# Optimization experiments

Measured on AMD Instinct MI355X. Metric: run time of the kernel, lower is better.

## Reference

```python
import jax, jax.numpy as jnp
import numpy as np

N_NODES = 50000
N_EDGES = 1_600_000
IN_C, HID_C, OUT_C = 512, 256, 50
ALPHA = 0.1
NUM_LAYERS = 10


def setup_inputs() -> dict:
    key = jax.random.key(0)
    ks = jax.random.split(key, 8)
    x = jax.random.normal(ks[0], (N_NODES, IN_C), dtype=jnp.float32)
    edge_row = jax.random.randint(ks[1], (N_EDGES,), 0, N_NODES, dtype=jnp.int32)
    edge_col = jax.random.randint(ks[2], (N_EDGES,), 0, N_NODES, dtype=jnp.int32)
    edge_weight = jax.random.uniform(ks[3], (N_EDGES,), dtype=jnp.float32)
    s1 = 1.0 / np.sqrt(IN_C)
    s2 = 1.0 / np.sqrt(HID_C)
    W1 = jax.random.uniform(ks[4], (IN_C, HID_C), minval=-s1, maxval=s1, dtype=jnp.float32)
    b1 = jax.random.uniform(ks[5], (HID_C,), minval=-s1, maxval=s1, dtype=jnp.float32)
    W2 = jax.random.uniform(ks[6], (HID_C, OUT_C), minval=-s2, maxval=s2, dtype=jnp.float32)
    b2 = jax.random.uniform(ks[7], (OUT_C,), minval=-s2, maxval=s2, dtype=jnp.float32)
    return {"x": x, "edge_row": edge_row, "edge_col": edge_col,
            "edge_weight": edge_weight, "W1": W1, "b1": b1, "W2": W2, "b2": b2}


def reference(x, edge_row, edge_col, edge_weight, W1, b1, W2, b2):
    # MLP: Linear -> ReLU -> Linear (dropout inactive in eval, no batch norm)
    h = jax.nn.relu(x @ W1 + b1)          # [N, HID_C]
    h = h @ W2 + b2                        # [N, OUT_C]
    x0 = h

    def spmm(v):
        # out[i] = sum_{e: row[e]==i} w[e] * v[col[e]]
        msgs = v[edge_col] * edge_weight[:, None]   # [E, OUT_C]
        return jax.ops.segment_sum(msgs, edge_row, num_segments=N_NODES)

    def step(h, _):
        h = spmm(h) * (1.0 - ALPHA) + ALPHA * x0
        return h, None

    h, _ = jax.lax.scan(step, h, None, length=NUM_LAYERS)
    return jax.nn.log_softmax(h, axis=1)
```

## Files before the change

kernel.cpp:

```cpp
#include <hip/hip_runtime.h>
#include <cstddef>
#include <cstdint>
#include <math.h>

#define N_NODES 50000
#define N_EDGES 1600000
#define IN_C 512
#define HID_C 256
#define OUT_C 50
#define PAD_C 64
#define NUM_LAYERS 10
#define NBUCK 98
#define BSHIFT 9
#define BCAP 20480
#define PHB_CHUNK 8192
#define PHB_BLOCKS 196

typedef __attribute__((ext_vector_type(8))) short short8;
typedef __attribute__((ext_vector_type(4))) float floatx4;

__device__ inline unsigned short f2bf(float f) {
    unsigned int u = __float_as_uint(f);
    u += 0x7fffu + ((u >> 16) & 1u);
    return (unsigned short)(u >> 16);
}

#define ASYNC16(g, l)                                                     \
    __builtin_amdgcn_global_load_lds(                                     \
        (const __attribute__((address_space(1))) void*)(g),               \
        (__attribute__((address_space(3))) void*)(l), 16, 0, 0)

__global__ __launch_bounds__(256) void transpose_w1(const float* __restrict__ W1,
                                                    unsigned short* __restrict__ Wt) {
    __shared__ float tile[32][33];
    int bx = blockIdx.x;
    int by = blockIdx.y;
    int tx = threadIdx.x & 31, ty = threadIdx.x >> 5;
#pragma unroll
    for (int i = 0; i < 32; i += 8)
        tile[ty + i][tx] = W1[(bx * 32 + ty + i) * HID_C + by * 32 + tx];
    __syncthreads();
#pragma unroll
    for (int i = 0; i < 32; i += 8)
        Wt[(size_t)(by * 32 + ty + i) * IN_C + bx * 32 + tx] = f2bf(tile[tx][ty + i]);
}

__global__ __launch_bounds__(256) void gemm1_mfma(const float* __restrict__ A,
                                                  const unsigned short* __restrict__ Wt,
                                                  const float* __restrict__ bias,
                                                  float* __restrict__ C) {
    __shared__ float          As[2][64 * 32];
    __shared__ unsigned short Bs[2][256 * 32];
    const int tid  = threadIdx.x;
    const int wave = tid >> 6, lane = tid & 63;
    const int quad = lane >> 4, l16 = lane & 15;
    const int m0 = blockIdx.x * 64;
    const int wm = (wave >> 1) * 32;
    const int wn = (wave & 1) * 128;

    floatx4 acc[2][8];
#pragma unroll
    for (int i = 0; i < 2; ++i)
#pragma unroll
        for (int j = 0; j < 8; ++j) acc[i][j] = (floatx4){0.f, 0.f, 0.f, 0.f};

    auto stage = [&](int buf, int k0) {
#pragma unroll
        for (int j = 0; j < 2; ++j) {
            int slot = tid + j * 256;
            int r = slot >> 3, c = slot & 7;
            int gr = m0 + r;
            if (gr >= N_NODES) gr = N_NODES - 1;
            const float* src = A + (size_t)gr * IN_C + k0 + ((c ^ (r & 7)) << 2);
            ASYNC16(src, &As[buf][slot << 2]);
        }
#pragma unroll
        for (int j = 0; j < 4; ++j) {
            int slot = tid + j * 256;
            int n = slot >> 2, c = slot & 3;
            const unsigned short* src = Wt + (size_t)n * IN_C + k0 + (c << 3);
            ASYNC16(src, &Bs[buf][slot << 3]);
        }
    };

    auto compute = [&](int buf) {
        short8 bfr[8], afr[2];
#pragma unroll
        for (int nt = 0; nt < 8; ++nt) {
            int n = wn + nt * 16 + l16;
            bfr[nt] = *(const short8*)&Bs[buf][(n << 5) + (quad << 3)];
        }
#pragma unroll
        for (int mt = 0; mt < 2; ++mt) {
            int r  = wm + mt * 16 + l16;
            int rx = r & 7;
            float4 lo = *(const float4*)&As[buf][(r << 5) + (((2 * quad)     ^ rx) << 2)];
            float4 hi = *(const float4*)&As[buf][(r << 5) + (((2 * quad + 1) ^ rx) << 2)];
            short8 a;
            a[0] = (short)f2bf(lo.x); a[1] = (short)f2bf(lo.y);
            a[2] = (short)f2bf(lo.z); a[3] = (short)f2bf(lo.w);
            a[4] = (short)f2bf(hi.x); a[5] = (short)f2bf(hi.y);
            a[6] = (short)f2bf(hi.z); a[7] = (short)f2bf(hi.w);
            afr[mt] = a;
        }
#pragma unroll
        for (int mt = 0; mt < 2; ++mt)
#pragma unroll
            for (int nt = 0; nt < 8; ++nt)
                acc[mt][nt] = __builtin_amdgcn_mfma_f32_16x16x32_bf16(afr[mt], bfr[nt],
                                                                      acc[mt][nt], 0, 0, 0);
    };

    stage(0, 0);
    __syncthreads();
    int buf = 0;
    for (int ks = 0; ks < IN_C / 32; ++ks) {
        if (ks + 1 < IN_C / 32) stage(buf ^ 1, (ks + 1) * 32);
        compute(buf);
        __syncthreads();
        buf ^= 1;
    }

#pragma unroll
    for (int nt = 0; nt < 8; ++nt) {
        int n = wn + nt * 16 + l16;
        float bn = bias[n];
#pragma unroll
        for (int mt = 0; mt < 2; ++mt) {
#pragma unroll
            for (int r = 0; r < 4; ++r) {
                int m = m0 + wm + mt * 16 + quad * 4 + r;
                if (m < N_NODES) {
                    float v = acc[mt][nt][r] + bn;
                    C[(size_t)m * HID_C + n] = v > 0.f ? v : 0.f;
                }
            }
        }
    }
}

__global__ void pad_w2(const float* __restrict__ W2, const float* __restrict__ b2,
                       float* __restrict__ Wp, float* __restrict__ bp) {
    int idx = blockIdx.x * blockDim.x + threadIdx.x;
    if (idx < HID_C * PAD_C) {
        int k = idx >> 6, j = idx & 63;
        Wp[idx] = (j < OUT_C) ? W2[k * OUT_C + j] : 0.f;
    }
    if (idx < PAD_C) bp[idx] = (idx < OUT_C) ? b2[idx] : 0.f;
}

__global__ __launch_bounds__(256) void gemm2_tiled(const float* __restrict__ H,
                                                   const float* __restrict__ Wp,
                                                   const float* __restrict__ bp,
                                                   float* __restrict__ h0f,
                                                   unsigned short* __restrict__ h0b) {
    __shared__ float As[16][68];
    __shared__ float Bs[16][64];
    const int tid = threadIdx.x;
    const int tx = tid & 15;
    const int ty = tid >> 4;
    const int m0 = blockIdx.x * 64;

    float acc[4][4];
#pragma unroll
    for (int i = 0; i < 4; ++i)
#pragma unroll
        for (int j = 0; j < 4; ++j) acc[i][j] = 0.f;

    const int arow = tid >> 2;
    const int akk  = (tid & 3) << 2;
    const int brow = tid >> 4;
    const int bcol = (tid & 15) << 2;

    for (int k0 = 0; k0 < HID_C; k0 += 16) {
        float4 av = make_float4(0.f, 0.f, 0.f, 0.f);
        int gr = m0 + arow;
        if (gr < N_NODES)
            av = *(const float4*)(H + (size_t)gr * HID_C + k0 + akk);
        As[akk + 0][arow] = av.x;
        As[akk + 1][arow] = av.y;
        As[akk + 2][arow] = av.z;
        As[akk + 3][arow] = av.w;
        float4 bv = *(const float4*)(Wp + (size_t)(k0 + brow) * PAD_C + bcol);
        *(float4*)&Bs[brow][bcol] = bv;
        __syncthreads();

#pragma unroll
        for (int kk = 0; kk < 16; ++kk) {
            float a[4], b[4];
#pragma unroll
            for (int i = 0; i < 4; ++i) a[i] = As[kk][ty * 4 + i];
#pragma unroll
            for (int j = 0; j < 4; ++j) b[j] = Bs[kk][tx * 4 + j];
#pragma unroll
            for (int i = 0; i < 4; ++i)
#pragma unroll
                for (int j = 0; j < 4; ++j) acc[i][j] = fmaf(a[i], b[j], acc[i][j]);
        }
        __syncthreads();
    }

#pragma unroll
    for (int i = 0; i < 4; ++i) {
        int r = m0 + ty * 4 + i;
        if (r >= N_NODES) continue;
#pragma unroll
        for (int j = 0; j < 4; ++j) {
            int c = tx * 4 + j;
            float v = acc[i][j] + bp[c];
            h0f[(size_t)r * PAD_C + c] = v;
            h0b[(size_t)r * PAD_C + c] = f2bf(v);
        }
    }
}

__global__ __launch_bounds__(256) void bucket_scatter(const int* __restrict__ erow,
                                                      const int* __restrict__ ecol,
                                                      const float* __restrict__ ew,
                                                      int* __restrict__ bfill,
                                                      uint2* __restrict__ buckets) {
    __shared__ int lcnt[NBUCK];
    __shared__ int lbase[NBUCK];
    const int t = threadIdx.x;
    for (int b = t; b < NBUCK; b += 256) lcnt[b] = 0;
    __syncthreads();
    const int e0 = blockIdx.x * PHB_CHUNK;
    const int e1 = min(e0 + PHB_CHUNK, N_EDGES);
    for (int e = e0 + t; e < e1; e += 256)
        atomicAdd(&lcnt[erow[e] >> BSHIFT], 1);
    __syncthreads();
    for (int b = t; b < NBUCK; b += 256) {
        lbase[b] = atomicAdd(&bfill[b], lcnt[b]);
        lcnt[b] = 0;
    }
    __syncthreads();
    for (int e = e0 + t; e < e1; e += 256) {
        int r = erow[e];
        int b = r >> BSHIFT;
        int o = atomicAdd(&lcnt[b], 1);
        int idx = lbase[b] + o;
        if (idx < BCAP) {
            unsigned packed = ((unsigned)(r - (b << BSHIFT)) << 17) | (unsigned)ecol[e];
            buckets[(size_t)b * BCAP + idx] = make_uint2(packed, __float_as_uint(ew[e]));
        }
    }
}

__global__ __launch_bounds__(128) void bucket_scan(const int* __restrict__ bfill,
                                                   int* __restrict__ bbase,
                                                   int* __restrict__ rowptr) {
    __shared__ int sd[128];
    int t = threadIdx.x;
    int v = (t < NBUCK) ? min(bfill[t], BCAP) : 0;
    sd[t] = v;
    __syncthreads();
    for (int off = 1; off < 128; off <<= 1) {
        int x = (t >= off) ? sd[t - off] : 0;
        __syncthreads();
        sd[t] += x;
        __syncthreads();
    }
    if (t < NBUCK) bbase[t] = sd[t] - v;
    if (t == NBUCK - 1) {
        bbase[NBUCK] = sd[t];
        rowptr[N_NODES] = sd[t];
    }
}

__global__ __launch_bounds__(256) void bucket_csr(const uint2* __restrict__ buckets,
                                                  const int* __restrict__ bfill,
                                                  const int* __restrict__ bbase,
                                                  int* __restrict__ rowptr,
                                                  uint2* __restrict__ edges) {
    __shared__ int hist[512];
    __shared__ int excl[512];
    __shared__ int psum[256];
    const int b = blockIdx.x;
    const int t = threadIdx.x;
    const int n = min(bfill[b], BCAP);
    const uint2* bk = buckets + (size_t)b * BCAP;

    hist[t] = 0; hist[t + 256] = 0;
    __syncthreads();
    for (int i = t; i < n; i += 256)
        atomicAdd(&hist[bk[i].x >> 17], 1);
    __syncthreads();
    int a0 = hist[2 * t], a1 = hist[2 * t + 1];
    psum[t] = a0 + a1;
    __syncthreads();
    for (int off = 1; off < 256; off <<= 1) {
        int x = (t >= off) ? psum[t - off] : 0;
        __syncthreads();
        psum[t] += x;
        __syncthreads();
    }
    int pe = psum[t] - (a0 + a1);
    excl[2 * t] = pe;
    excl[2 * t + 1] = pe + a0;
    __syncthreads();
    const int base = bbase[b];
#pragma unroll
    for (int k = 0; k < 2; ++k) {
        int lr = t + k * 256;
        int r = (b << BSHIFT) + lr;
        if (r < N_NODES) rowptr[r] = base + excl[lr];
    }
    hist[t] = 0; hist[t + 256] = 0;
    __syncthreads();
    for (int i = t; i < n; i += 256) {
        uint2 ed = bk[i];
        int lr = ed.x >> 17;
        int pos = base + excl[lr] + atomicAdd(&hist[lr], 1);
        edges[pos] = make_uint2(ed.x & 0x1FFFFu, ed.y);
    }
}

template <bool LAST>
__global__ __launch_bounds__(256) void prop8(const int* __restrict__ rowptr,
                                             const uint2* __restrict__ edges,
                                             const unsigned short* __restrict__ hin,
                                             const float* __restrict__ h0f,
                                             unsigned short* __restrict__ hout_b,
                                             float* __restrict__ out_f) {
    int wid = (blockIdx.x * blockDim.x + threadIdx.x) >> 6;
    if (wid >= N_NODES) return;
    int lane = threadIdx.x & 63;
    int slot = lane >> 3;
    int lc   = lane & 7;
    int s = rowptr[wid], e = rowptr[wid + 1];

    float acc0[8], acc1[8];
#pragma unroll
    for (int k = 0; k < 8; ++k) { acc0[k] = 0.f; acc1[k] = 0.f; }

    int i = s;
    for (; i + 16 <= e; i += 16) {
        uint2 cw0 = edges[i + slot];
        uint2 cw1 = edges[i + 8 + slot];
        uint4 hv0 = *(const uint4*)((const char*)hin + ((size_t)cw0.x << 7) + lc * 16);
        uint4 hv1 = *(const uint4*)((const char*)hin + ((size_t)cw1.x << 7) + lc * 16);
        float w0 = __uint_as_float(cw0.y);
        float w1 = __uint_as_float(cw1.y);
        acc0[0] = fmaf(w0, __uint_as_float(hv0.x << 16),         acc0[0]);
        acc0[1] = fmaf(w0, __uint_as_float(hv0.x & 0xffff0000u), acc0[1]);
        acc0[2] = fmaf(w0, __uint_as_float(hv0.y << 16),         acc0[2]);
        acc0[3] = fmaf(w0, __uint_as_float(hv0.y & 0xffff0000u), acc0[3]);
        acc0[4] = fmaf(w0, __uint_as_float(hv0.z << 16),         acc0[4]);
        acc0[5] = fmaf(w0, __uint_as_float(hv0.z & 0xffff0000u), acc0[5]);
        acc0[6] = fmaf(w0, __uint_as_float(hv0.w << 16),         acc0[6]);
        acc0[7] = fmaf(w0, __uint_as_float(hv0.w & 0xffff0000u), acc0[7]);
        acc1[0] = fmaf(w1, __uint_as_float(hv1.x << 16),         acc1[0]);
        acc1[1] = fmaf(w1, __uint_as_float(hv1.x & 0xffff0000u), acc1[1]);
        acc1[2] = fmaf(w1, __uint_as_float(hv1.y << 16),         acc1[2]);
        acc1[3] = fmaf(w1, __uint_as_float(hv1.y & 0xffff0000u), acc1[3]);
        acc1[4] = fmaf(w1, __uint_as_float(hv1.z << 16),         acc1[4]);
        acc1[5] = fmaf(w1, __uint_as_float(hv1.z & 0xffff0000u), acc1[5]);
        acc1[6] = fmaf(w1, __uint_as_float(hv1.w << 16),         acc1[6]);
        acc1[7] = fmaf(w1, __uint_as_float(hv1.w & 0xffff0000u), acc1[7]);
    }
    for (; i < e; i += 8) {
        int idx = i + slot;
        uint2 cw = (idx < e) ? edges[idx] : make_uint2(0u, 0u);
        float w  = (idx < e) ? __uint_as_float(cw.y) : 0.f;
        uint4 hv = *(const uint4*)((const char*)hin + ((size_t)cw.x << 7) + lc * 16);
        acc0[0] = fmaf(w, __uint_as_float(hv.x << 16),         acc0[0]);
        acc0[1] = fmaf(w, __uint_as_float(hv.x & 0xffff0000u), acc0[1]);
        acc0[2] = fmaf(w, __uint_as_float(hv.y << 16),         acc0[2]);
        acc0[3] = fmaf(w, __uint_as_float(hv.y & 0xffff0000u), acc0[3]);
        acc0[4] = fmaf(w, __uint_as_float(hv.z << 16),         acc0[4]);
        acc0[5] = fmaf(w, __uint_as_float(hv.z & 0xffff0000u), acc0[5]);
        acc0[6] = fmaf(w, __uint_as_float(hv.w << 16),         acc0[6]);
        acc0[7] = fmaf(w, __uint_as_float(hv.w & 0xffff0000u), acc0[7]);
    }

    float r[8];
#pragma unroll
    for (int k = 0; k < 8; ++k) {
        float v = acc0[k] + acc1[k];
        v += __shfl_xor(v, 8, 64);
        v += __shfl_xor(v, 16, 64);
        v += __shfl_xor(v, 32, 64);
        r[k] = v;
    }

    size_t off = (size_t)wid * PAD_C + lc * 8;
    float4 h0a = *(const float4*)(h0f + off);
    float4 h0b4 = *(const float4*)(h0f + off + 4);
    r[0] = 0.9f * r[0] + 0.1f * h0a.x;  r[1] = 0.9f * r[1] + 0.1f * h0a.y;
    r[2] = 0.9f * r[2] + 0.1f * h0a.z;  r[3] = 0.9f * r[3] + 0.1f * h0a.w;
    r[4] = 0.9f * r[4] + 0.1f * h0b4.x; r[5] = 0.9f * r[5] + 0.1f * h0b4.y;
    r[6] = 0.9f * r[6] + 0.1f * h0b4.z; r[7] = 0.9f * r[7] + 0.1f * h0b4.w;

    if (!LAST) {
        if (slot == 0) {
            uint4 u;
            u.x = ((unsigned)f2bf(r[1]) << 16) | f2bf(r[0]);
            u.y = ((unsigned)f2bf(r[3]) << 16) | f2bf(r[2]);
            u.z = ((unsigned)f2bf(r[5]) << 16) | f2bf(r[4]);
            u.w = ((unsigned)f2bf(r[7]) << 16) | f2bf(r[6]);
            *(uint4*)((char*)hout_b + ((size_t)wid << 7) + lc * 16) = u;
        }
    } else {
        int ch0 = lc * 8;
        float m = -INFINITY;
#pragma unroll
        for (int k = 0; k < 8; ++k) if (ch0 + k < OUT_C) m = fmaxf(m, r[k]);
        m = fmaxf(m, __shfl_xor(m, 1, 64));
        m = fmaxf(m, __shfl_xor(m, 2, 64));
        m = fmaxf(m, __shfl_xor(m, 4, 64));
        float ss = 0.f;
#pragma unroll
        for (int k = 0; k < 8; ++k) if (ch0 + k < OUT_C) ss += __expf(r[k] - m);
        ss += __shfl_xor(ss, 1, 64);
        ss += __shfl_xor(ss, 2, 64);
        ss += __shfl_xor(ss, 4, 64);
        float lse = __logf(ss);
        if (slot == 0) {
#pragma unroll
            for (int k = 0; k < 8; ++k)
                if (ch0 + k < OUT_C)
                    out_f[(size_t)wid * OUT_C + ch0 + k] = (r[k] - m) - lse;
        }
    }
}

extern "C" void kernel_launch(void* const* d_in, const int* in_sizes, int n_in,
                              void* d_out, int out_size, void* d_ws, size_t ws_size,
                              hipStream_t stream) {
    const float* x    = (const float*)d_in[0];
    const int*   erow = (const int*)d_in[1];
    const int*   ecol = (const int*)d_in[2];
    const float* ew   = (const float*)d_in[3];
    const float* W1   = (const float*)d_in[4];
    const float* b1   = (const float*)d_in[5];
    const float* W2   = (const float*)d_in[6];
    const float* b2   = (const float*)d_in[7];
    float* out = (float*)d_out;

    char* p = (char*)d_ws;
    auto alloc = [&](size_t bytes) {
        char* r = p;
        p += (bytes + 255) & ~(size_t)255;
        return r;
    };
    char*  h_hid_raw = alloc((size_t)N_NODES * HID_C * 4);
    float* h_hid  = (float*)h_hid_raw;
    float* h0f    = (float*)alloc((size_t)N_NODES * PAD_C * 4);
    unsigned short* h0b = (unsigned short*)alloc((size_t)N_NODES * PAD_C * 2);
    uint2* edges  = (uint2*)alloc((size_t)N_EDGES * 8);
    int*   rowptr = (int*)alloc((size_t)(N_NODES + 1) * 4);
    int*   bfill  = (int*)alloc((size_t)NBUCK * 4);
    int*   bbase  = (int*)alloc((size_t)(NBUCK + 1) * 4);
    float* Wp     = (float*)alloc((size_t)HID_C * PAD_C * 4);
    float* bp     = (float*)alloc((size_t)PAD_C * 4);
    unsigned short* Wt = (unsigned short*)alloc((size_t)HID_C * IN_C * 2);
    uint2* buckets = (uint2*)h_hid_raw;
    unsigned short* ha = (unsigned short*)h_hid_raw;
    unsigned short* hb = (unsigned short*)(h_hid_raw + (size_t)N_NODES * PAD_C * 2);

    hipMemsetAsync(bfill, 0, (size_t)NBUCK * 4, stream);

    bucket_scatter<<<PHB_BLOCKS, 256, 0, stream>>>(erow, ecol, ew, bfill, buckets);
    bucket_scan<<<1, 128, 0, stream>>>(bfill, bbase, rowptr);
    bucket_csr<<<NBUCK, 256, 0, stream>>>(buckets, bfill, bbase, rowptr, edges);

    transpose_w1<<<dim3(IN_C / 32, HID_C / 32), 256, 0, stream>>>(W1, Wt);
    gemm1_mfma<<<dim3((N_NODES + 63) / 64), 256, 0, stream>>>(x, Wt, b1, h_hid);
    pad_w2<<<(HID_C * PAD_C + 255) / 256, 256, 0, stream>>>(W2, b2, Wp, bp);
    gemm2_tiled<<<(N_NODES + 63) / 64, 256, 0, stream>>>(h_hid, Wp, bp, h0f, h0b);

    const int prop_blocks = (N_NODES * 64 + 255) / 256;
    const unsigned short* cur = h0b;
    unsigned short* nxt = ha;
    for (int l = 0; l < NUM_LAYERS - 1; ++l) {
        prop8<false><<<prop_blocks, 256, 0, stream>>>(rowptr, edges, cur, h0f,
                                                      nxt, nullptr);
        const unsigned short* t = nxt;
        nxt = (nxt == ha) ? hb : ha;
        cur = t;
    }
    prop8<true><<<prop_blocks, 256, 0, stream>>>(rowptr, edges, cur, h0f,
                                                 nullptr, out);
}
```

Before: 645.8 us.

## Fuse second linear layer into MFMA GEMM1 and restructure LDS pipeline

```diff
diff --git a/kernel.cpp b/kernel.cpp
--- a/kernel.cpp
+++ b/kernel.cpp
@@ -30,6 +30,11 @@
         (const __attribute__((address_space(1))) void*)(g),               \
         (__attribute__((address_space(3))) void*)(l), 16, 0, 0)
 
+#define WAITCNT6() asm volatile("s_waitcnt vmcnt(6)" ::: "memory")
+#define WAITCNT0() asm volatile("s_waitcnt vmcnt(0)" ::: "memory")
+#define SBAR()     __builtin_amdgcn_s_barrier()
+#define SFENCE()   __builtin_amdgcn_sched_barrier(0)
+
 __global__ __launch_bounds__(256) void transpose_w1(const float* __restrict__ W1,
                                                     unsigned short* __restrict__ Wt) {
     __shared__ float tile[32][33];
@@ -45,12 +50,32 @@
         Wt[(size_t)(by * 32 + ty + i) * IN_C + bx * 32 + tx] = f2bf(tile[tx][ty + i]);
 }
 
-__global__ __launch_bounds__(256) void gemm1_mfma(const float* __restrict__ A,
-                                                  const unsigned short* __restrict__ Wt,
-                                                  const float* __restrict__ bias,
-                                                  float* __restrict__ C) {
-    __shared__ float          As[2][64 * 32];
-    __shared__ unsigned short Bs[2][256 * 32];
+__global__ void pad_w2(const float* __restrict__ W2, const float* __restrict__ b2,
+                       unsigned short* __restrict__ Wpt, float* __restrict__ bp) {
+    int idx = blockIdx.x * blockDim.x + threadIdx.x;
+    if (idx < PAD_C * HID_C) {
+        int n = idx >> 8, k = idx & 255;
+        float v = (n < OUT_C) ? W2[k * OUT_C + n] : 0.f;
+        Wpt[idx] = f2bf(v);
+    }
+    if (idx < PAD_C) bp[idx] = (idx < OUT_C) ? b2[idx] : 0.f;
+}
+
+__global__ __launch_bounds__(256) void gemm1_fused(const float* __restrict__ A,
+                                                   const unsigned short* __restrict__ Wt,
+                                                   const float* __restrict__ b1,
+                                                   const unsigned short* __restrict__ Wpt,
+                                                   const float* __restrict__ bp,
+                                                   float* __restrict__ h0f,
+                                                   unsigned short* __restrict__ h0b) {
+    __shared__ __align__(16) char smem[49152];
+    float*          As0 = (float*)smem;
+    float*          As1 = (float*)(smem + 8192);
+    unsigned short* Bs0 = (unsigned short*)(smem + 16384);
+    unsigned short* Bs1 = (unsigned short*)(smem + 32768);
+    unsigned short* Hs  = (unsigned short*)smem;
+    const int HS_LD = 264;
+
     const int tid  = threadIdx.x;
     const int wave = tid >> 6, lane = tid & 63;
     const int quad = lane >> 4, l16 = lane & 15;
@@ -64,7 +89,7 @@
 #pragma unroll
         for (int j = 0; j < 8; ++j) acc[i][j] = (floatx4){0.f, 0.f, 0.f, 0.f};
 
-    auto stage = [&](int buf, int k0) {
+    auto stage = [&](float* As_, unsigned short* Bs_, int k0) {
 #pragma unroll
         for (int j = 0; j < 2; ++j) {
             int slot = tid + j * 256;
@@ -72,30 +97,28 @@
             int gr = m0 + r;
             if (gr >= N_NODES) gr = N_NODES - 1;
             const float* src = A + (size_t)gr * IN_C + k0 + ((c ^ (r & 7)) << 2);
-            ASYNC16(src, &As[buf][slot << 2]);
+            ASYNC16(src, As_ + (slot << 2));
         }
 #pragma unroll
         for (int j = 0; j < 4; ++j) {
-            int slot = tid + j * 256;
-            int n = slot >> 2, c = slot & 3;
-            const unsigned short* src = Wt + (size_t)n * IN_C + k0 + (c << 3);
-            ASYNC16(src, &Bs[buf][slot << 3]);
+            const unsigned short* src = Wt + (size_t)tid * IN_C + k0 + (j << 3);
+            ASYNC16(src, Bs_ + (j << 11) + (tid << 3));
         }
     };
 
-    auto compute = [&](int buf) {
+    auto compute = [&](const float* As_, const unsigned short* Bs_) {
         short8 bfr[8], afr[2];
 #pragma unroll
         for (int nt = 0; nt < 8; ++nt) {
             int n = wn + nt * 16 + l16;
-            bfr[nt] = *(const short8*)&Bs[buf][(n << 5) + (quad << 3)];
+            bfr[nt] = *(const short8*)&Bs_[(quad << 11) + (n << 3)];
         }
 #pragma unroll
         for (int mt = 0; mt < 2; ++mt) {
             int r  = wm + mt * 16 + l16;
             int rx = r & 7;
-            float4 lo = *(const float4*)&As[buf][(r << 5) + (((2 * quad)     ^ rx) << 2)];
-            float4 hi = *(const float4*)&As[buf][(r << 5) + (((2 * quad + 1) ^ rx) << 2)];
+            float4 lo = *(const float4*)&As_[(r << 5) + (((2 * quad)     ^ rx) << 2)];
+            float4 hi = *(const float4*)&As_[(r << 5) + (((2 * quad + 1) ^ rx) << 2)];
             short8 a;
             a[0] = (short)f2bf(lo.x); a[1] = (short)f2bf(lo.y);
             a[2] = (short)f2bf(lo.z); a[3] = (short)f2bf(lo.w);
@@ -111,105 +134,65 @@
                                                                       acc[mt][nt], 0, 0, 0);
     };
 
-    stage(0, 0);
-    __syncthreads();
-    int buf = 0;
-    for (int ks = 0; ks < IN_C / 32; ++ks) {
-        if (ks + 1 < IN_C / 32) stage(buf ^ 1, (ks + 1) * 32);
-        compute(buf);
-        __syncthreads();
-        buf ^= 1;
-    }
+    stage(As0, Bs0, 0);
+    stage(As1, Bs1, 32);
+    WAITCNT6(); SFENCE(); SBAR(); SFENCE();
+    for (int kk = 0; kk < 7; ++kk) {
+        compute(As0, Bs0);
+        SFENCE(); SBAR(); SFENCE();
+        stage(As0, Bs0, (2 * kk + 2) * 32);
+        WAITCNT6(); SFENCE(); SBAR(); SFENCE();
+        compute(As1, Bs1);
+        SFENCE(); SBAR(); SFENCE();
+        stage(As1, Bs1, (2 * kk + 3) * 32);
+        WAITCNT6(); SFENCE(); SBAR(); SFENCE();
+    }
+    compute(As0, Bs0);
+    SFENCE(); SBAR(); SFENCE();
+    WAITCNT0(); SFENCE(); SBAR(); SFENCE();
+    compute(As1, Bs1);
+    __syncthreads();
 
 #pragma unroll
     for (int nt = 0; nt < 8; ++nt) {
         int n = wn + nt * 16 + l16;
-        float bn = bias[n];
-#pragma unroll
-        for (int mt = 0; mt < 2; ++mt) {
+        float bn = b1[n];
+#pragma unroll
+        for (int mt = 0; mt < 2; ++mt)
 #pragma unroll
             for (int r = 0; r < 4; ++r) {
-                int m = m0 + wm + mt * 16 + quad * 4 + r;
-                if (m < N_NODES) {
-                    float v = acc[mt][nt][r] + bn;
-                    C[(size_t)m * HID_C + n] = v > 0.f ? v : 0.f;
-                }
+                float v = acc[mt][nt][r] + bn;
+                v = v > 0.f ? v : 0.f;
+                Hs[(wm + mt * 16 + quad * 4 + r) * HS_LD + n] = f2bf(v);
             }
-        }
-    }
-}
-
-__global__ void pad_w2(const float* __restrict__ W2, const float* __restrict__ b2,
-                       float* __restrict__ Wp, float* __restrict__ bp) {
-    int idx = blockIdx.x * blockDim.x + threadIdx.x;
-    if (idx < HID_C * PAD_C) {
-        int k = idx >> 6, j = idx & 63;
-        Wp[idx] = (j < OUT_C) ? W2[k * OUT_C + j] : 0.f;
-    }
-    if (idx < PAD_C) bp[idx] = (idx < OUT_C) ? b2[idx] : 0.f;
-}
-
-__global__ __launch_bounds__(256) void gemm2_tiled(const float* __restrict__ H,
-                                                   const float* __restrict__ Wp,
-                                                   const float* __restrict__ bp,
-                                                   float* __restrict__ h0f,
-                                                   unsigned short* __restrict__ h0b) {
-    __shared__ float As[16][68];
-    __shared__ float Bs[16][64];
-    const int tid = threadIdx.x;
-    const int tx = tid & 15;
-    const int ty = tid >> 4;
-    const int m0 = blockIdx.x * 64;
-
-    float acc[4][4];
-#pragma unroll
-    for (int i = 0; i < 4; ++i)
-#pragma unroll
-        for (int j = 0; j < 4; ++j) acc[i][j] = 0.f;
-
-    const int arow = tid >> 2;
-    const int akk  = (tid & 3) << 2;
-    const int brow = tid >> 4;
-    const int bcol = (tid & 15) << 2;
-
-    for (int k0 = 0; k0 < HID_C; k0 += 16) {
-        float4 av = make_float4(0.f, 0.f, 0.f, 0.f);
-        int gr = m0 + arow;
-        if (gr < N_NODES)
-            av = *(const float4*)(H + (size_t)gr * HID_C + k0 + akk);
-        As[akk + 0][arow] = av.x;
-        As[akk + 1][arow] = av.y;
-        As[akk + 2][arow] = av.z;
-        As[akk + 3][arow] = av.w;
-        float4 bv = *(const float4*)(Wp + (size_t)(k0 + brow) * PAD_C + bcol);
-        *(float4*)&Bs[brow][bcol] = bv;
-        __syncthreads();
-
-#pragma unroll
-        for (int kk = 0; kk < 16; ++kk) {
-            float a[4], b[4];
-#pragma unroll
-            for (int i = 0; i < 4; ++i) a[i] = As[kk][ty * 4 + i];
-#pragma unroll
-            for (int j = 0; j < 4; ++j) b[j] = Bs[kk][tx * 4 + j];
-#pragma unroll
-            for (int i = 0; i < 4; ++i)
-#pragma unroll
-                for (int j = 0; j < 4; ++j) acc[i][j] = fmaf(a[i], b[j], acc[i][j]);
-        }
-        __syncthreads();
-    }
-
-#pragma unroll
-    for (int i = 0; i < 4; ++i) {
-        int r = m0 + ty * 4 + i;
-        if (r >= N_NODES) continue;
-#pragma unroll
-        for (int j = 0; j < 4; ++j) {
-            int c = tx * 4 + j;
-            float v = acc[i][j] + bp[c];
-            h0f[(size_t)r * PAD_C + c] = v;
-            h0b[(size_t)r * PAD_C + c] = f2bf(v);
+    }
+    __syncthreads();
+
+    floatx4 acc2[4];
+#pragma unroll
+    for (int nt = 0; nt < 4; ++nt) acc2[nt] = (floatx4){0.f, 0.f, 0.f, 0.f};
+    const int hrow = (wave << 4) + l16;
+#pragma unroll
+    for (int k2 = 0; k2 < 8; ++k2) {
+        short8 haf = *(const short8*)&Hs[hrow * HS_LD + (k2 << 5) + (quad << 3)];
+#pragma unroll
+        for (int nt = 0; nt < 4; ++nt) {
+            short8 bf = *(const short8*)&Wpt[(size_t)((nt << 4) + l16) * HID_C + (k2 << 5) + (quad << 3)];
+            acc2[nt] = __builtin_amdgcn_mfma_f32_16x16x32_bf16(haf, bf, acc2[nt], 0, 0, 0);
+        }
+    }
+#pragma unroll
+    for (int nt = 0; nt < 4; ++nt) {
+        int c = (nt << 4) + l16;
+        float bn = bp[c];
+#pragma unroll
+        for (int r = 0; r < 4; ++r) {
+            int row = m0 + (wave << 4) + (quad << 2) + r;
+            if (row < N_NODES) {
+                float v = acc2[nt][r] + bn;
+                h0f[(size_t)row * PAD_C + c] = v;
+                h0b[(size_t)row * PAD_C + c] = f2bf(v);
+            }
         }
     }
 }
@@ -443,20 +426,19 @@
         p += (bytes + 255) & ~(size_t)255;
         return r;
     };
-    char*  h_hid_raw = alloc((size_t)N_NODES * HID_C * 4);
-    float* h_hid  = (float*)h_hid_raw;
+    char*  scratch = alloc((size_t)NBUCK * BCAP * 8);
     float* h0f    = (float*)alloc((size_t)N_NODES * PAD_C * 4);
     unsigned short* h0b = (unsigned short*)alloc((size_t)N_NODES * PAD_C * 2);
     uint2* edges  = (uint2*)alloc((size_t)N_EDGES * 8);
     int*   rowptr = (int*)alloc((size_t)(N_NODES + 1) * 4);
     int*   bfill  = (int*)alloc((size_t)NBUCK * 4);
     int*   bbase  = (int*)alloc((size_t)(NBUCK + 1) * 4);
-    float* Wp     = (float*)alloc((size_t)HID_C * PAD_C * 4);
     float* bp     = (float*)alloc((size_t)PAD_C * 4);
-    unsigned short* Wt = (unsigned short*)alloc((size_t)HID_C * IN_C * 2);
-    uint2* buckets = (uint2*)h_hid_raw;
-    unsigned short* ha = (unsigned short*)h_hid_raw;
-    unsigned short* hb = (unsigned short*)(h_hid_raw + (size_t)N_NODES * PAD_C * 2);
+    unsigned short* Wt  = (unsigned short*)alloc((size_t)HID_C * IN_C * 2);
+    unsigned short* Wpt = (unsigned short*)alloc((size_t)PAD_C * HID_C * 2);
+    uint2* buckets = (uint2*)scratch;
+    unsigned short* ha = (unsigned short*)scratch;
+    unsigned short* hb = (unsigned short*)(scratch + (size_t)N_NODES * PAD_C * 2);
 
     hipMemsetAsync(bfill, 0, (size_t)NBUCK * 4, stream);
 
@@ -465,9 +447,8 @@
     bucket_csr<<<NBUCK, 256, 0, stream>>>(buckets, bfill, bbase, rowptr, edges);
 
     transpose_w1<<<dim3(IN_C / 32, HID_C / 32), 256, 0, stream>>>(W1, Wt);
-    gemm1_mfma<<<dim3((N_NODES + 63) / 64), 256, 0, stream>>>(x, Wt, b1, h_hid);
-    pad_w2<<<(HID_C * PAD_C + 255) / 256, 256, 0, stream>>>(W2, b2, Wp, bp);
-    gemm2_tiled<<<(N_NODES + 63) / 64, 256, 0, stream>>>(h_hid, Wp, bp, h0f, h0b);
+    pad_w2<<<(PAD_C * HID_C + 255) / 256, 256, 0, stream>>>(W2, b2, Wpt, bp);
+    gemm1_fused<<<(N_NODES + 63) / 64, 256, 0, stream>>>(x, Wt, b1, Wpt, bp, h0f, h0b);
 
     const int prop_blocks = (N_NODES * 64 + 255) / 256;
     const unsigned short* cur = h0b;
```

Measured after the change: 631.8 us. 1.02x faster.
